# Kernel tuning notes

Measured on AMD Instinct MI355X. Metric: run time of the kernel, lower is better.

## Reference

```python
import jax, jax.numpy as jnp
import numpy as np

B, N, QD = 1, 4096, 1024
H, DH = 16, 64  # heads, dim_head; inner_dim = H*DH = 1024
SCALE = DH ** -0.5


def setup_inputs() -> dict:
    key = jax.random.key(0)
    ks = jax.random.split(key, 6)
    inner = H * DH
    return {
        "x": jax.random.normal(ks[0], (B, N, QD), dtype=jnp.float32),
        "Wq": jax.random.normal(ks[1], (QD, inner), dtype=jnp.float32) * (QD ** -0.5),
        "Wk": jax.random.normal(ks[2], (QD, inner), dtype=jnp.float32) * (QD ** -0.5),
        "Wv": jax.random.normal(ks[3], (QD, inner), dtype=jnp.float32) * (QD ** -0.5),
        "Wo": jax.random.normal(ks[4], (inner, QD), dtype=jnp.float32) * (inner ** -0.5),
        "bo": jnp.zeros((QD,), dtype=jnp.float32),
    }


def reference(x, Wq, Wk, Wv, Wo, bo):
    b, n, _ = x.shape
    # projections, split heads: b n (h d) -> b h n d
    q = (x @ Wq).reshape(b, n, H, DH).transpose(0, 2, 1, 3)
    k = (x @ Wk).reshape(b, n, H, DH).transpose(0, 2, 1, 3)
    v = (x @ Wv).reshape(b, n, H, DH).transpose(0, 2, 1, 3)
    # fp32-forced QK^T (ATTN_PRECISION='fp32' path), then scale
    sim = jnp.einsum("bhid,bhjd->bhij", q.astype(jnp.float32), k.astype(jnp.float32)) * SCALE
    attn = jax.nn.softmax(sim, axis=-1)
    out = jnp.einsum("bhij,bhjd->bhid", attn, v)  # b h n d
    out = out.transpose(0, 2, 1, 3).reshape(b, n, H * DH)  # merge heads
    return out @ Wo + bo
```

## Files before the change

### kernel.cpp

```cpp
#include <hip/hip_runtime.h>
#include <stdint.h>

#define NH 16
#define NN 4096

typedef __attribute__((ext_vector_type(8))) short bf16x8;
typedef __attribute__((ext_vector_type(4))) short bf16x4;
typedef __attribute__((ext_vector_type(4))) float f32x4;
typedef __attribute__((ext_vector_type(16))) float f32x16;
typedef unsigned short u16;
typedef unsigned int u32;
typedef __attribute__((ext_vector_type(4))) u32 u32x4;

__device__ __forceinline__ u16 f2bf(float f) {
  u32 u = __float_as_uint(f);
  return (u16)((u + 0x7FFFu + ((u >> 16) & 1u)) >> 16);
}

#define GLD16(gp, lp)                                              \
  __builtin_amdgcn_global_load_lds(                                \
      (__attribute__((address_space(1))) void*)(gp),               \
      (__attribute__((address_space(3))) void*)(lp), 16, 0, 0)

__global__ __launch_bounds__(256) void cvt_bf16_kernel(const float* __restrict__ src,
                                                       u16* __restrict__ dst, int n) {
  int i = (blockIdx.x * blockDim.x + threadIdx.x) * 8;
  if (i >= n) return;
  float4 a = *(const float4*)(src + i);
  float4 b = *(const float4*)(src + i + 4);
  uint4 o;
  o.x = (u32)f2bf(a.x) | ((u32)f2bf(a.y) << 16);
  o.y = (u32)f2bf(a.z) | ((u32)f2bf(a.w) << 16);
  o.z = (u32)f2bf(b.x) | ((u32)f2bf(b.y) << 16);
  o.w = (u32)f2bf(b.z) | ((u32)f2bf(b.w) << 16);
  *(uint4*)(dst + i) = o;
}

__global__ __launch_bounds__(256) void transpose4(const float* __restrict__ Wq,
                                                  const float* __restrict__ Wk,
                                                  const float* __restrict__ Wv,
                                                  const float* __restrict__ Wo,
                                                  u16* __restrict__ Wqt, u16* __restrict__ Wkt,
                                                  u16* __restrict__ Wvt, u16* __restrict__ Wot) {
  __shared__ float tile[64][65];
  const float* src;
  u16* dst;
  float scale = 1.0f;
  int z = blockIdx.z;
  if (z == 0) { src = Wq; dst = Wqt; scale = 0.125f * 1.4426950408889634f; }
  else if (z == 1) { src = Wk; dst = Wkt; }
  else if (z == 2) { src = Wv; dst = Wvt; }
  else { src = Wo; dst = Wot; }
  int tx = threadIdx.x & 63, ty = threadIdx.x >> 6;
  int c0 = blockIdx.x * 64, r0 = blockIdx.y * 64;
#pragma unroll
  for (int i = ty; i < 64; i += 4)
    tile[i][tx] = src[(size_t)(r0 + i) * 1024 + c0 + tx];
  __syncthreads();
#pragma unroll
  for (int i = ty; i < 64; i += 4)
    dst[(size_t)(c0 + i) * 1024 + r0 + tx] = f2bf(tile[tx][i] * scale);
}

__global__ __launch_bounds__(256) void gemm_qkv(const u16* __restrict__ A,
                                                const u16* __restrict__ Bt,
                                                u16* __restrict__ Qb, u16* __restrict__ Kb,
                                                u16* __restrict__ Vth) {
  __shared__ __align__(16) u16 A_lds[2][128 * 32];
  __shared__ __align__(16) u16 B_lds[2][128 * 32];
  const int tid = threadIdx.x;
  const int l = tid & 63, w = tid >> 6;
  const int g = l >> 4, c = l & 15;
  const int wr = w >> 1, wc = w & 1;
  const int m0 = blockIdx.y * 128, n0 = blockIdx.x * 128;

  const int srow = tid >> 2;
  const u32 sswz = (u32)(((tid & 3) * 16) ^ ((srow & 3) << 4));
  const char* Ag = (const char*)A + (size_t)(m0 + srow) * 2048 + sswz;
  const char* Bg = (const char*)Bt + (size_t)(n0 + srow) * 2048 + sswz;
  const u32 ldsb = (u32)(w * 1024);

#define GSTAGE(buf, ks_)                                                          \
  do {                                                                            \
    u32 koff_ = (u32)(ks_) * 64;                                                  \
    _Pragma("unroll") for (int p_ = 0; p_ < 2; ++p_) {                            \
      GLD16(Ag + koff_ + (size_t)p_ * 64 * 2048,                                  \
            (char*)A_lds[buf] + p_ * 4096 + ldsb);                                \
      GLD16(Bg + koff_ + (size_t)p_ * 64 * 2048,                                  \
            (char*)B_lds[buf] + p_ * 4096 + ldsb);                                \
    }                                                                             \
  } while (0)

  f32x4 acc[4][4];
#pragma unroll
  for (int i = 0; i < 4; ++i)
#pragma unroll
    for (int j = 0; j < 4; ++j) acc[i][j] = (f32x4){0.f, 0.f, 0.f, 0.f};

  int cur = 0;
  GSTAGE(0, 0);
  for (int ks = 0; ks < 32; ++ks) {
    GSTAGE(cur ^ 1, (ks + 1) & 31);
    asm volatile("s_waitcnt vmcnt(4)" ::: "memory");
    __builtin_amdgcn_s_barrier();
    __builtin_amdgcn_sched_barrier(0);
    const char* Ac = (const char*)A_lds[cur];
    const char* Bc = (const char*)B_lds[cur];
    bf16x8 af[4], bfr[4];
#pragma unroll
    for (int i = 0; i < 4; ++i) {
      int row = wr * 64 + i * 16 + c;
      af[i] = *(const bf16x8*)(Ac + row * 64 + ((g * 16) ^ ((row & 3) << 4)));
    }
#pragma unroll
    for (int j = 0; j < 4; ++j) {
      int row = wc * 64 + j * 16 + c;
      bfr[j] = *(const bf16x8*)(Bc + row * 64 + ((g * 16) ^ ((row & 3) << 4)));
    }
    __builtin_amdgcn_s_setprio(1);
#pragma unroll
    for (int i = 0; i < 4; ++i)
#pragma unroll
      for (int j = 0; j < 4; ++j)
        acc[i][j] = __builtin_amdgcn_mfma_f32_16x16x32_bf16(af[i], bfr[j], acc[i][j], 0, 0, 0);
    __builtin_amdgcn_s_setprio(0);
    asm volatile("s_waitcnt lgkmcnt(0)" ::: "memory");
    __builtin_amdgcn_s_barrier();
    __builtin_amdgcn_sched_barrier(0);
    cur ^= 1;
  }
#undef GSTAGE

  const int sec = n0 >> 10;
#pragma unroll
  for (int i = 0; i < 4; ++i)
#pragma unroll
    for (int j = 0; j < 4; ++j)
#pragma unroll
      for (int r = 0; r < 4; ++r) {
        int m = m0 + wr * 64 + i * 16 + g * 4 + r;
        int col = n0 + wc * 64 + j * 16 + c;
        int cc = col & 1023;
        u16 v = f2bf(acc[i][j][r]);
        if (sec == 0) Qb[(size_t)m * 1024 + cc] = v;
        else if (sec == 1) Kb[(size_t)m * 1024 + cc] = v;
        else Vth[(size_t)cc * 4096 + m] = v;
      }
}

__global__ __launch_bounds__(256) void gemm_out64(const u16* __restrict__ A,
                                                  const u16* __restrict__ Bt,
                                                  float* __restrict__ out,
                                                  const float* __restrict__ bias) {
  __shared__ __align__(16) u16 A_lds[2][64 * 32];
  __shared__ __align__(16) u16 B_lds[2][64 * 32];
  const int tid = threadIdx.x;
  const int l = tid & 63, w = tid >> 6;
  const int g = l >> 4, c = l & 15;
  const int wr = w >> 1, wc = w & 1;
  const int m0 = blockIdx.y * 64, n0 = blockIdx.x * 64;

  const int srow = tid >> 2;
  const u32 sswz = (u32)(((tid & 3) * 16) ^ ((srow & 3) << 4));
  const char* Ag = (const char*)A + (size_t)(m0 + srow) * 2048 + sswz;
  const char* Bg = (const char*)Bt + (size_t)(n0 + srow) * 2048 + sswz;
  const u32 ldsb = (u32)(w * 1024);

#define GSTAGE2(buf, ks_)                                                         \
  do {                                                                            \
    u32 koff_ = (u32)(ks_) * 64;                                                  \
    GLD16(Ag + koff_, (char*)A_lds[buf] + ldsb);                                  \
    GLD16(Bg + koff_, (char*)B_lds[buf] + ldsb);                                  \
  } while (0)

  f32x4 acc[2][2];
#pragma unroll
  for (int i = 0; i < 2; ++i)
#pragma unroll
    for (int j = 0; j < 2; ++j) acc[i][j] = (f32x4){0.f, 0.f, 0.f, 0.f};

  int cur = 0;
  GSTAGE2(0, 0);
  for (int ks = 0; ks < 32; ++ks) {
    GSTAGE2(cur ^ 1, (ks + 1) & 31);
    asm volatile("s_waitcnt vmcnt(2)" ::: "memory");
    __builtin_amdgcn_s_barrier();
    __builtin_amdgcn_sched_barrier(0);
    const char* Ac = (const char*)A_lds[cur];
    const char* Bc = (const char*)B_lds[cur];
    bf16x8 af[2], bfr[2];
#pragma unroll
    for (int i = 0; i < 2; ++i) {
      int row = wr * 32 + i * 16 + c;
      af[i] = *(const bf16x8*)(Ac + row * 64 + ((g * 16) ^ ((row & 3) << 4)));
    }
#pragma unroll
    for (int j = 0; j < 2; ++j) {
      int row = wc * 32 + j * 16 + c;
      bfr[j] = *(const bf16x8*)(Bc + row * 64 + ((g * 16) ^ ((row & 3) << 4)));
    }
    __builtin_amdgcn_s_setprio(1);
#pragma unroll
    for (int i = 0; i < 2; ++i)
#pragma unroll
      for (int j = 0; j < 2; ++j)
        acc[i][j] = __builtin_amdgcn_mfma_f32_16x16x32_bf16(af[i], bfr[j], acc[i][j], 0, 0, 0);
    __builtin_amdgcn_s_setprio(0);
    asm volatile("s_waitcnt lgkmcnt(0)" ::: "memory");
    __builtin_amdgcn_s_barrier();
    __builtin_amdgcn_sched_barrier(0);
    cur ^= 1;
  }
#undef GSTAGE2

#pragma unroll
  for (int i = 0; i < 2; ++i)
#pragma unroll
    for (int j = 0; j < 2; ++j)
#pragma unroll
      for (int r = 0; r < 4; ++r) {
        int m = m0 + wr * 32 + i * 16 + g * 4 + r;
        int col = n0 + wc * 32 + j * 16 + c;
        out[(size_t)m * 1024 + col] = acc[i][j][r] + bias[col];
      }
}

__global__ __launch_bounds__(256) void flash_attn(const u16* __restrict__ Qb,
                                                  const u16* __restrict__ Kb,
                                                  const u16* __restrict__ Vt,
                                                  u16* __restrict__ Ob) {
  __shared__ __align__(16) u16 K_lds[2][64 * 64];
  __shared__ __align__(16) u16 V_lds[2][64 * 64];
  const int tid = threadIdx.x;
  const int l = tid & 63, w = tid >> 6;
  const int lq = l & 31, hi = l >> 5;
  const int h = blockIdx.y;
  const int q = blockIdx.x * 128 + w * 32 + lq;

  bf16x8 qf[4];
  const u16* qrow = Qb + (size_t)q * 1024 + h * 64;
#pragma unroll
  for (int dm = 0; dm < 4; ++dm) qf[dm] = *(const bf16x8*)(qrow + dm * 16 + hi * 8);

  f32x16 ot[2];
#pragma unroll
  for (int a = 0; a < 2; ++a)
#pragma unroll
    for (int r = 0; r < 16; ++r) ot[a][r] = 0.f;
  float lrow = 0.f;
  f32x16 stA[2], stB[2];

  const int srow = tid >> 3;
  const u32 sswz = (u32)(((tid & 7) * 16) ^ ((srow & 7) << 4));
  const char* Kg = (const char*)Kb + ((size_t)srow * 1024 + h * 64) * 2 + sswz;
  const char* Vg = (const char*)Vt + ((size_t)(h * 64 + srow) * 4096) * 2 + sswz;
  const u32 ldsb = (u32)(w * 1024);

#define CONSUME(STP, VSLOT)                                                       \
  {                                                                               \
    const char* Vp_ = (const char*)(VSLOT);                                       \
    u32 pk[16];                                                                   \
    float rsum = 0.f;                                                             \
    _Pragma("unroll") for (int s_ = 0; s_ < 2; ++s_)                              \
    _Pragma("unroll") for (int j_ = 0; j_ < 8; ++j_) {                            \
      float p0_ = __builtin_amdgcn_exp2f(STP[s_][2 * j_]);                        \
      float p1_ = __builtin_amdgcn_exp2f(STP[s_][2 * j_ + 1]);                    \
      rsum += p0_ + p1_;                                                          \
      u32 wpk_;                                                                   \
      asm("v_cvt_pk_bf16_f32 %0, %1, %2" : "=v"(wpk_) : "v"(p0_), "v"(p1_));      \
      pk[s_ * 8 + j_] = wpk_;                                                     \
    }                                                                             \
    lrow += rsum;                                                                 \
    __builtin_amdgcn_s_setprio(1);                                                \
    _Pragma("unroll") for (int sti_ = 0; sti_ < 4; ++sti_) {                      \
      u32x4 pw_ = {pk[sti_ * 4 + 0], pk[sti_ * 4 + 1], pk[sti_ * 4 + 2],          \
                   pk[sti_ * 4 + 3]};                                             \
      bf16x8 pfrag_ = __builtin_bit_cast(bf16x8, pw_);                            \
      const u32 cb_ = (u32)(sti_ * 32 + hi * 8);                                  \
      _Pragma("unroll") for (int a_ = 0; a_ < 2; ++a_) {                          \
        const int rowd_ = a_ * 32 + lq;                                           \
        const u32 rs_ = (u32)(rowd_ * 128), rz_ = (u32)((rowd_ & 7) << 4);        \
        bf16x4 v0_ = *(const bf16x4*)(Vp_ + rs_ + (cb_ ^ rz_));                   \
        bf16x4 v1_ = *(const bf16x4*)(Vp_ + rs_ + ((cb_ + 16) ^ rz_));            \
        bf16x8 vf_ = __builtin_shufflevector(v0_, v1_, 0, 1, 2, 3, 4, 5, 6, 7);   \
        ot[a_] = __builtin_amdgcn_mfma_f32_32x32x16_bf16(vf_, pfrag_, ot[a_], 0, 0, 0); \
      }                                                                           \
    }                                                                             \
    __builtin_amdgcn_s_setprio(0);                                                \
  }

#define BODY(TI, STC, STP, DOPREV)                                                \
  {                                                                               \
    const int ti_ = (TI);                                                         \
    const int nxt_ = (ti_ + 1) & 63;                                              \
    {                                                                             \
      const char* kg_ = Kg + (size_t)nxt_ * 64 * 2048;                            \
      char* kl_ = (char*)K_lds[nxt_ & 1] + ldsb;                                  \
      GLD16(kg_, kl_);                                                            \
      GLD16(kg_ + 32 * 2048, kl_ + 4096);                                         \
      const char* vg_ = Vg + (size_t)ti_ * 128;                                   \
      char* vl_ = (char*)V_lds[ti_ & 1] + ldsb;                                   \
      GLD16(vg_, vl_);                                                            \
      GLD16(vg_ + (size_t)32 * 8192, vl_ + 4096);                                 \
    }                                                                             \
    asm volatile("s_waitcnt vmcnt(4)" ::: "memory");                              \
    __builtin_amdgcn_s_barrier();                                                 \
    __builtin_amdgcn_sched_barrier(0);                                            \
    const char* Kc_ = (const char*)K_lds[ti_ & 1];                                \
    _Pragma("unroll") for (int s_ = 0; s_ < 2; ++s_)                              \
    _Pragma("unroll") for (int r_ = 0; r_ < 16; ++r_) STC[s_][r_] = 0.f;          \
    __builtin_amdgcn_s_setprio(1);                                                \
    _Pragma("unroll") for (int s_ = 0; s_ < 2; ++s_) {                            \
      const int row_ = s_ * 32 + lq;                                              \
      const u32 rs_ = (u32)(row_ * 128), rz_ = (u32)((row_ & 7) << 4);            \
      _Pragma("unroll") for (int dm_ = 0; dm_ < 4; ++dm_) {                       \
        bf16x8 kf_ = *(const bf16x8*)(Kc_ + rs_ + ((u32)(dm_ * 32 + hi * 16) ^ rz_)); \
        STC[s_] = __builtin_amdgcn_mfma_f32_32x32x16_bf16(kf_, qf[dm_], STC[s_], 0, 0, 0); \
      }                                                                           \
    }                                                                             \
    __builtin_amdgcn_s_setprio(0);                                                \
    if (DOPREV) CONSUME(STP, V_lds[(ti_ - 1) & 1]);                               \
    asm volatile("s_waitcnt lgkmcnt(0)" ::: "memory");                            \
    __builtin_amdgcn_s_barrier();                                                 \
    __builtin_amdgcn_sched_barrier(0);                                            \
  }

  {
    char* kl = (char*)K_lds[0] + ldsb;
    GLD16(Kg, kl);
    GLD16(Kg + 32 * 2048, kl + 4096);
  }

  BODY(0, stA, stA, 0);
  for (int i = 1; i < 63; i += 2) {
    BODY(i, stB, stA, 1);
    BODY(i + 1, stA, stB, 1);
  }
  BODY(63, stB, stA, 1);
  asm volatile("s_waitcnt vmcnt(0)" ::: "memory");
  __builtin_amdgcn_s_barrier();
  __builtin_amdgcn_sched_barrier(0);
  CONSUME(stB, V_lds[1]);

#undef BODY
#undef CONSUME

  lrow += __shfl_xor(lrow, 32, 64);
  float inv = 1.f / lrow;
  u16* orow = Ob + (size_t)q * 1024 + h * 64 + hi * 4;
#pragma unroll
  for (int a = 0; a < 2; ++a)
#pragma unroll
    for (int rr = 0; rr < 4; ++rr) {
      ushort4 o4;
      o4.x = f2bf(ot[a][rr * 4 + 0] * inv);
      o4.y = f2bf(ot[a][rr * 4 + 1] * inv);
      o4.z = f2bf(ot[a][rr * 4 + 2] * inv);
      o4.w = f2bf(ot[a][rr * 4 + 3] * inv);
      *(ushort4*)(orow + a * 32 + rr * 8) = o4;
    }
}

extern "C" void kernel_launch(void* const* d_in, const int* in_sizes, int n_in,
                              void* d_out, int out_size, void* d_ws, size_t ws_size,
                              hipStream_t stream) {
  const float* x = (const float*)d_in[0];
  const float* Wq = (const float*)d_in[1];
  const float* Wk = (const float*)d_in[2];
  const float* Wv = (const float*)d_in[3];
  const float* Wo = (const float*)d_in[4];
  const float* bo = (const float*)d_in[5];
  float* out = (float*)d_out;

  char* ws = (char*)d_ws;
  u16* xb  = (u16*)(ws);
  u16* Wqt = (u16*)(ws + (8u << 20));
  u16* Wkt = (u16*)(ws + (10u << 20));
  u16* Wvt = (u16*)(ws + (12u << 20));
  u16* Wot = (u16*)(ws + (14u << 20));
  u16* Qb  = (u16*)(ws + (16u << 20));
  u16* Kbf = (u16*)(ws + (24u << 20));
  u16* Vth = (u16*)(ws + (32u << 20));
  u16* Ob  = (u16*)(ws + (40u << 20));

  cvt_bf16_kernel<<<2048, 256, 0, stream>>>(x, xb, 4096 * 1024);
  transpose4<<<dim3(16, 16, 4), 256, 0, stream>>>(Wq, Wk, Wv, Wo, Wqt, Wkt, Wvt, Wot);
  gemm_qkv<<<dim3(24, 32), 256, 0, stream>>>(xb, Wqt, Qb, Kbf, Vth);
  flash_attn<<<dim3(32, 16), 256, 0, stream>>>(Qb, Kbf, Vth, Ob);
  gemm_out64<<<dim3(16, 64), 256, 0, stream>>>(Ob, Wot, out, bo);
}
```

Before: 196.8 us.

## Split flash attention over two KV halves and merge partials in a separate kernel

The attention kernel is templated so each head/query tile can be split along the key sequence into two halves, doubling the grid through a z dimension. Each half writes unnormalised fp32 partial outputs and row sums to workspace. A new merge kernel adds the halves, normalises and converts to bf16 before the output GEMM. The aim is more parallel blocks and better latency hiding on the GPU, at the cost of extra fp32 global traffic, another launch, and a path that only runs when the workspace is large enough.

```diff
diff --git a/kernel.cpp b/kernel.cpp
--- a/kernel.cpp
+++ b/kernel.cpp
@@ -225,16 +225,22 @@
       }
 }
 
-__global__ __launch_bounds__(256) void flash_attn(const u16* __restrict__ Qb,
-                                                  const u16* __restrict__ Kb,
-                                                  const u16* __restrict__ Vt,
-                                                  u16* __restrict__ Ob) {
+template <int SPLIT>
+__global__ __launch_bounds__(256) void flash_attn_t(const u16* __restrict__ Qb,
+                                                    const u16* __restrict__ Kb,
+                                                    const u16* __restrict__ Vt,
+                                                    u16* __restrict__ Ob,
+                                                    float* __restrict__ Op,
+                                                    float* __restrict__ Lp) {
+  constexpr int NT = SPLIT ? 32 : 64;
   __shared__ __align__(16) u16 K_lds[2][64 * 64];
   __shared__ __align__(16) u16 V_lds[2][64 * 64];
   const int tid = threadIdx.x;
   const int l = tid & 63, w = tid >> 6;
   const int lq = l & 31, hi = l >> 5;
   const int h = blockIdx.y;
+  const int z = SPLIT ? blockIdx.z : 0;
+  const int kb = z * 32;
   const int q = blockIdx.x * 128 + w * 32 + lq;
 
   bf16x8 qf[4];
@@ -292,13 +298,13 @@
 #define BODY(TI, STC, STP, DOPREV)                                                \
   {                                                                               \
     const int ti_ = (TI);                                                         \
-    const int nxt_ = (ti_ + 1) & 63;                                              \
+    const int nxt_ = (ti_ + 1) & (NT - 1);                                        \
     {                                                                             \
-      const char* kg_ = Kg + (size_t)nxt_ * 64 * 2048;                            \
+      const char* kg_ = Kg + (size_t)(kb + nxt_) * 64 * 2048;                     \
       char* kl_ = (char*)K_lds[nxt_ & 1] + ldsb;                                  \
       GLD16(kg_, kl_);                                                            \
       GLD16(kg_ + 32 * 2048, kl_ + 4096);                                         \
-      const char* vg_ = Vg + (size_t)ti_ * 128;                                   \
+      const char* vg_ = Vg + (size_t)(kb + ti_) * 128;                            \
       char* vl_ = (char*)V_lds[ti_ & 1] + ldsb;                                   \
       GLD16(vg_, vl_);                                                            \
       GLD16(vg_ + (size_t)32 * 8192, vl_ + 4096);                                 \
@@ -326,39 +332,79 @@
   }
 
   {
+    const char* kg0 = Kg + (size_t)kb * 64 * 2048;
     char* kl = (char*)K_lds[0] + ldsb;
-    GLD16(Kg, kl);
-    GLD16(Kg + 32 * 2048, kl + 4096);
+    GLD16(kg0, kl);
+    GLD16(kg0 + 32 * 2048, kl + 4096);
   }
 
   BODY(0, stA, stA, 0);
-  for (int i = 1; i < 63; i += 2) {
+  for (int i = 1; i < NT - 1; i += 2) {
     BODY(i, stB, stA, 1);
     BODY(i + 1, stA, stB, 1);
   }
-  BODY(63, stB, stA, 1);
+  BODY(NT - 1, stB, stA, 1);
   asm volatile("s_waitcnt vmcnt(0)" ::: "memory");
   __builtin_amdgcn_s_barrier();
   __builtin_amdgcn_sched_barrier(0);
-  CONSUME(stB, V_lds[1]);
+  CONSUME(stB, V_lds[(NT - 1) & 1]);
 
 #undef BODY
 #undef CONSUME
 
   lrow += __shfl_xor(lrow, 32, 64);
-  float inv = 1.f / lrow;
-  u16* orow = Ob + (size_t)q * 1024 + h * 64 + hi * 4;
-#pragma unroll
-  for (int a = 0; a < 2; ++a)
-#pragma unroll
-    for (int rr = 0; rr < 4; ++rr) {
-      ushort4 o4;
-      o4.x = f2bf(ot[a][rr * 4 + 0] * inv);
-      o4.y = f2bf(ot[a][rr * 4 + 1] * inv);
-      o4.z = f2bf(ot[a][rr * 4 + 2] * inv);
-      o4.w = f2bf(ot[a][rr * 4 + 3] * inv);
-      *(ushort4*)(orow + a * 32 + rr * 8) = o4;
-    }
+  if constexpr (SPLIT) {
+    float* orow = Op + (size_t)z * (4096 * 1024) + (size_t)q * 1024 + h * 64 + hi * 4;
+#pragma unroll
+    for (int a = 0; a < 2; ++a)
+#pragma unroll
+      for (int rr = 0; rr < 4; ++rr) {
+        float4 fv = {ot[a][rr * 4 + 0], ot[a][rr * 4 + 1], ot[a][rr * 4 + 2],
+                     ot[a][rr * 4 + 3]};
+        *(float4*)(orow + a * 32 + rr * 8) = fv;
+      }
+    if (hi == 0) Lp[z * 65536 + h * 4096 + q] = lrow;
+  } else {
+    float inv = 1.f / lrow;
+    u16* orow = Ob + (size_t)q * 1024 + h * 64 + hi * 4;
+#pragma unroll
+    for (int a = 0; a < 2; ++a)
+#pragma unroll
+      for (int rr = 0; rr < 4; ++rr) {
+        ushort4 o4;
+        o4.x = f2bf(ot[a][rr * 4 + 0] * inv);
+        o4.y = f2bf(ot[a][rr * 4 + 1] * inv);
+        o4.z = f2bf(ot[a][rr * 4 + 2] * inv);
+        o4.w = f2bf(ot[a][rr * 4 + 3] * inv);
+        *(ushort4*)(orow + a * 32 + rr * 8) = o4;
+      }
+  }
+}
+
+__global__ __launch_bounds__(256) void merge_halves(const float* __restrict__ O0,
+                                                    const float* __restrict__ O1,
+                                                    const float* __restrict__ L0,
+                                                    const float* __restrict__ L1,
+                                                    u16* __restrict__ Ob) {
+  int idx = blockIdx.x * 256 + threadIdx.x;
+  int q = idx >> 7;
+  int c0 = (idx & 127) * 8;
+  int h = c0 >> 6;
+  float inv = 1.f / (L0[h * 4096 + q] + L1[h * 4096 + q]);
+  size_t off = (size_t)q * 1024 + c0;
+  float4 a0 = *(const float4*)(O0 + off), a1 = *(const float4*)(O0 + off + 4);
+  float4 b0 = *(const float4*)(O1 + off), b1 = *(const float4*)(O1 + off + 4);
+  ushort4 o0, o1;
+  o0.x = f2bf((a0.x + b0.x) * inv);
+  o0.y = f2bf((a0.y + b0.y) * inv);
+  o0.z = f2bf((a0.z + b0.z) * inv);
+  o0.w = f2bf((a0.w + b0.w) * inv);
+  o1.x = f2bf((a1.x + b1.x) * inv);
+  o1.y = f2bf((a1.y + b1.y) * inv);
+  o1.z = f2bf((a1.z + b1.z) * inv);
+  o1.w = f2bf((a1.w + b1.w) * inv);
+  *(ushort4*)(Ob + off) = o0;
+  *(ushort4*)(Ob + off + 4) = o1;
 }
 
 extern "C" void kernel_launch(void* const* d_in, const int* in_sizes, int n_in,
@@ -375,17 +421,29 @@
   char* ws = (char*)d_ws;
   u16* xb  = (u16*)(ws);
   u16* Wqt = (u16*)(ws + (8u << 20));
-  u16* Wkt = (u16*)(ws + (10u << 20));
-  u16* Wvt = (u16*)(ws + (12u << 20));
   u16* Wot = (u16*)(ws + (14u << 20));
   u16* Qb  = (u16*)(ws + (16u << 20));
   u16* Kbf = (u16*)(ws + (24u << 20));
   u16* Vth = (u16*)(ws + (32u << 20));
   u16* Ob  = (u16*)(ws + (40u << 20));
+  float* Op = (float*)(ws + (40u << 20));
+  float* Lp = (float*)(ws + (72u << 20));
+  u16* Wkt = Wqt + (1u << 20);
+  u16* Wvt = Wqt + (2u << 20);
+
+  const bool split = ws_size >= ((73u << 20) + (1u << 19));
 
   cvt_bf16_kernel<<<2048, 256, 0, stream>>>(x, xb, 4096 * 1024);
   transpose4<<<dim3(16, 16, 4), 256, 0, stream>>>(Wq, Wk, Wv, Wo, Wqt, Wkt, Wvt, Wot);
   gemm_qkv<<<dim3(24, 32), 256, 0, stream>>>(xb, Wqt, Qb, Kbf, Vth);
-  flash_attn<<<dim3(32, 16), 256, 0, stream>>>(Qb, Kbf, Vth, Ob);
-  gemm_out64<<<dim3(16, 64), 256, 0, stream>>>(Ob, Wot, out, bo);
-}
+
+  if (split) {
+    flash_attn_t<1><<<dim3(32, 16, 2), 256, 0, stream>>>(Qb, Kbf, Vth, nullptr, Op, Lp);
+    u16* ObM = (u16*)ws;
+    merge_halves<<<2048, 256, 0, stream>>>(Op, Op + (1u << 22), Lp, Lp + 65536, ObM);
+    gemm_out64<<<dim3(16, 64), 256, 0, stream>>>(ObM, Wot, out, bo);
+  } else {
+    flash_attn_t<0><<<dim3(32, 16, 1), 256, 0, stream>>>(Qb, Kbf, Vth, Ob, nullptr, nullptr);
+    gemm_out64<<<dim3(16, 64), 256, 0, stream>>>(Ob, Wot, out, bo);
+  }
+}
```

After: 207.8 us. 5.6% more time.
